# Kernel optimization log

Hardware: AMD Instinct MI355X
Metric: run time of the kernel (lower is better)

The kernel has to match this reference:

```python
import jax, jax.numpy as jnp
import numpy as np

# Instant-NGP multi-resolution hash grid constants (match init_kwargs)
L = 16            # num_levels
F = 2             # level_dim (features per level)
LOG2T = 19
T = 1 << LOG2T    # hashmap entries per level
BASE = 16.0       # base_resolution
SCALE = 1.3819061 # per_level_scale
HIDDEN = 64
N = 500_000
P1 = jnp.uint32(2654435761)  # NGP spatial hash primes (prime for dim0 is 1)
P2 = jnp.uint32(805459861)
# 8 corner offsets of the voxel, [8,3]
OFFS = jnp.array([[i, j, k] for i in (0, 1) for j in (0, 1) for k in (0, 1)], dtype=jnp.float32)


def hash_encode(x, table):
    # x: [N,3] in [0,1];  table: [L,T,F]
    res = jnp.floor(BASE * SCALE ** jnp.arange(L, dtype=jnp.float32))   # [L]
    pos = x[None] * (res[:, None, None] - 1.0)                          # [L,N,3]
    p0 = jnp.floor(pos)
    f = pos - p0                                                        # trilinear fracs [L,N,3]
    pi = p0.astype(jnp.uint32)                                          # [L,N,3]
    offs_u = OFFS.astype(jnp.uint32)                                    # [8,3]
    cx = pi[..., 0:1] + offs_u[None, None, :, 0]                        # [L,N,8]
    cy = pi[..., 1:2] + offs_u[None, None, :, 1]
    cz = pi[..., 2:3] + offs_u[None, None, :, 2]
    idx = (cx ^ (cy * P1) ^ (cz * P2)) & jnp.uint32(T - 1)              # [L,N,8] hashed table index
    feats = jax.vmap(lambda tab, i: tab[i])(table, idx)                 # per-level gather -> [L,N,8,F]
    # trilinear weights: prod over dims of (f if corner bit set else 1-f)
    w = jnp.prod(jnp.where(OFFS[None, None] > 0.5, f[:, :, None, :], 1.0 - f[:, :, None, :]), axis=-1)  # [L,N,8]
    out = jnp.einsum('lnc,lncf->lnf', w, feats)                         # [L,N,F]
    return out.transpose(1, 0, 2).reshape(x.shape[0], L * F)           # [N, L*F]


def setup_inputs() -> dict:
    key = jax.random.key(0)
    k = jax.random.split(key, 8)
    x = jax.random.uniform(k[0], (N, 3), dtype=jnp.float32)
    # NGP-style small uniform init for the hash tables
    table = jax.random.normal(k[1], (L, T, F), dtype=jnp.float32) * 1e-4
    feat_dim = L * F
    w1 = jax.random.normal(k[2], (feat_dim, HIDDEN), dtype=jnp.float32) / np.sqrt(feat_dim)
    b1 = jnp.zeros((HIDDEN,), jnp.float32)
    w2 = jax.random.normal(k[3], (HIDDEN, HIDDEN), dtype=jnp.float32) / np.sqrt(HIDDEN)
    b2 = jnp.zeros((HIDDEN,), jnp.float32)
    w3 = jax.random.normal(k[4], (HIDDEN, 3), dtype=jnp.float32) / np.sqrt(HIDDEN)
    b3 = jnp.zeros((3,), jnp.float32)
    return {"x": x, "table": table, "w1": w1, "b1": b1, "w2": w2, "b2": b2, "w3": w3, "b3": b3}


def reference(x, table, w1, b1, w2, b2, w3, b3):
    feat = hash_encode(x, table)                         # [N, 32]
    h = jax.nn.relu(feat @ w1 + b1)
    h = jax.nn.relu(h @ w2 + b2)
    rgb = jax.nn.sigmoid(h @ w3 + b3)                    # [N, 3]
    return rgb
```

## Files before the change

kernel.cpp:

```cpp
#include <hip/hip_runtime.h>
#include <hip/hip_fp16.h>
#include <math.h>


constexpr int      LVLS   = 16;
constexpr uint32_t TSIZE  = 1u << 19;
constexpr uint32_t TMASK  = TSIZE - 1u;
constexpr uint32_t PRIME1 = 2654435761u;
constexpr uint32_t PRIME2 = 805459861u;

struct ResArr { float v[LVLS]; };

typedef __attribute__((ext_vector_type(8))) short short8v;
typedef __attribute__((ext_vector_type(4))) float float4v;

__device__ inline ushort f2bf(float f) {
    uint u = __float_as_uint(f);
    u += 0x7fffu + ((u >> 16) & 1u);
    return (ushort)(u >> 16);
}

__device__ inline float2 h2f(uint u) {
    __half2 h = *reinterpret_cast<__half2*>(&u);
    return __half22float2(h);
}

__device__ inline uint pick4(const uint4& b, uint j) {
    const uint lo = (j & 1u) ? b.y : b.x;
    const uint hi = (j & 1u) ? b.w : b.z;
    return (j & 2u) ? hi : lo;
}

__global__ __launch_bounds__(256)
void ingp_conv(const float* __restrict__ table, uint* __restrict__ tab16,
               const float* __restrict__ x, float4* __restrict__ x4, int n)
{
    const int t = blockIdx.x * 256 + threadIdx.x;
    const int HALF = LVLS * (int)TSIZE / 2;
    if (t < HALF) {
        const float4 v = *reinterpret_cast<const float4*>(table + (size_t)t * 4u);
        __half2 ha = __floats2half2_rn(v.x, v.y);
        __half2 hb = __floats2half2_rn(v.z, v.w);
        uint2 o;
        o.x = *reinterpret_cast<uint*>(&ha);
        o.y = *reinterpret_cast<uint*>(&hb);
        *reinterpret_cast<uint2*>(tab16 + (size_t)t * 2u) = o;
    }
    if (t < n)
        x4[t] = make_float4(x[3 * t + 0], x[3 * t + 1], x[3 * t + 2], 0.f);
}

__global__ __launch_bounds__(256)
void ingp_prep(const float* __restrict__ w1, const float* __restrict__ w2,
               const float* __restrict__ w3,
               ushort* __restrict__ w1t, ushort* __restrict__ w2t,
               ushort* __restrict__ w3t)
{
    const int t = blockIdx.x * 256 + threadIdx.x;
    if (t < 2048) {
        const int nn = t >> 5, k = t & 31;
        w1t[t] = f2bf(w1[k * 64 + nn]);
    } else if (t < 2048 + 4096) {
        const int q = t - 2048;
        const int nn = q >> 6, k = q & 63;
        w2t[q] = f2bf(w2[k * 64 + nn]);
    } else if (t < 2048 + 4096 + 1024) {
        const int q = t - 6144;
        const int nn = q >> 6, k = q & 63;
        w3t[q] = (nn < 3) ? f2bf(w3[k * 3 + nn]) : (ushort)0;
    }
}

__global__ __launch_bounds__(256, 8)
void ingp_encode_f16(const float4* __restrict__ x4,
                     const uint* __restrict__ tab16,
                     uint* __restrict__ feat, int n, ResArr res)
{
    const int i = blockIdx.x * 256 + threadIdx.x;
    const int l = blockIdx.y;
    if (i >= n) return;

    const float4 xp = x4[i];
    const float rm1 = res.v[l];
    const float px = xp.x * rm1, py = xp.y * rm1, pz = xp.z * rm1;
    const float fpx = floorf(px), fpy = floorf(py), fpz = floorf(pz);
    const float fx = px - fpx, fy = py - fpy, fz = pz - fpz;
    const uint32_t ix = (uint32_t)fpx;
    const uint32_t iy = (uint32_t)fpy;
    const uint32_t iz = (uint32_t)fpz;
    const uint32_t hy0 = iy * PRIME1, hy1 = (iy + 1u) * PRIME1;
    const uint32_t hz0 = iz * PRIME2, hz1 = (iz + 1u) * PRIME2;
    const uint* tl = tab16 + (size_t)l * (size_t)TSIZE;

    uint32_t h0[4], h1[4];
    #pragma unroll
    for (int p = 0; p < 4; ++p) {
        const uint32_t bj = (p >> 1) & 1, bk = p & 1;
        const uint32_t hyz = (bj ? hy1 : hy0) ^ (bk ? hz1 : hz0);
        h0[p] = (ix ^ hyz) & TMASK;
        h1[p] = ((ix + 1u) ^ hyz) & TMASK;
    }

    uint e0[4], e1[4];
    if ((ix & 3u) != 3u) {
        #pragma unroll
        for (int p = 0; p < 4; ++p) {
            const uint32_t base = h0[p] & ~3u;
            const uint4 blk = *reinterpret_cast<const uint4*>(tl + base);
            e0[p] = pick4(blk, h0[p] & 3u);
            e1[p] = pick4(blk, h1[p] & 3u);
        }
    } else {
        #pragma unroll
        for (int p = 0; p < 4; ++p) {
            e0[p] = tl[h0[p]];
            e1[p] = tl[h1[p]];
        }
    }

    const float gx0 = 1.f - fx, gx1 = fx;
    float a0 = 0.f, a1 = 0.f;
    #pragma unroll
    for (int p = 0; p < 4; ++p) {
        const int bj = (p >> 1) & 1, bk = p & 1;
        const float wyz = (bj ? fy : 1.f - fy) * (bk ? fz : 1.f - fz);
        const float w0 = wyz * gx0, w1 = wyz * gx1;
        const float2 c0 = h2f(e0[p]);
        const float2 c1 = h2f(e1[p]);
        a0 = fmaf(w0, c0.x, a0);
        a1 = fmaf(w0, c0.y, a1);
        a0 = fmaf(w1, c1.x, a0);
        a1 = fmaf(w1, c1.y, a1);
    }
    feat[(size_t)l * n + i] = (uint)f2bf(a0) | ((uint)f2bf(a1) << 16);
}

__global__ __launch_bounds__(256, 8)
void ingp_encode(const float* __restrict__ x,
                 const float* __restrict__ table,
                 uint* __restrict__ feat, int n, ResArr res)
{
    const int i = blockIdx.x * 256 + threadIdx.x;
    const int l = blockIdx.y;
    if (i >= n) return;
    const float xx = x[3 * i + 0], xy = x[3 * i + 1], xz = x[3 * i + 2];
    const float rm1 = res.v[l];
    const float px = xx * rm1, py = xy * rm1, pz = xz * rm1;
    const float fpx = floorf(px), fpy = floorf(py), fpz = floorf(pz);
    const float fx = px - fpx, fy = py - fpy, fz = pz - fpz;
    const uint32_t ix = (uint32_t)fpx, iy = (uint32_t)fpy, iz = (uint32_t)fpz;
    const uint32_t hy0 = iy * PRIME1, hy1 = (iy + 1u) * PRIME1;
    const uint32_t hz0 = iz * PRIME2, hz1 = (iz + 1u) * PRIME2;
    const float* tl = table + (size_t)l * (size_t)TSIZE * 2u;

    uint32_t idx0[4], idx1[4];
    #pragma unroll
    for (int p = 0; p < 4; ++p) {
        const uint32_t bj = (p >> 1) & 1, bk = p & 1;
        const uint32_t hyz = (bj ? hy1 : hy0) ^ (bk ? hz1 : hz0);
        idx0[p] = (ix ^ hyz) & TMASK;
        idx1[p] = ((ix + 1u) ^ hyz) & TMASK;
    }
    float2 c0[4], c1[4];
    if ((ix & 1u) == 0u) {
        #pragma unroll
        for (int p = 0; p < 4; ++p) {
            const uint32_t base = idx0[p] & ~1u;
            const float4 q = *reinterpret_cast<const float4*>(tl + (size_t)base * 2u);
            if (idx0[p] & 1u) { c0[p] = make_float2(q.z, q.w); c1[p] = make_float2(q.x, q.y); }
            else              { c0[p] = make_float2(q.x, q.y); c1[p] = make_float2(q.z, q.w); }
        }
    } else {
        #pragma unroll
        for (int p = 0; p < 4; ++p) {
            c0[p] = *reinterpret_cast<const float2*>(tl + (size_t)idx0[p] * 2u);
            c1[p] = *reinterpret_cast<const float2*>(tl + (size_t)idx1[p] * 2u);
        }
    }
    const float gx0 = 1.f - fx, gx1 = fx;
    float a0 = 0.f, a1 = 0.f;
    #pragma unroll
    for (int p = 0; p < 4; ++p) {
        const int bj = (p >> 1) & 1, bk = p & 1;
        const float wyz = (bj ? fy : 1.f - fy) * (bk ? fz : 1.f - fz);
        const float w0 = wyz * gx0, w1 = wyz * gx1;
        a0 = fmaf(w0, c0[p].x, a0);
        a1 = fmaf(w0, c0[p].y, a1);
        a0 = fmaf(w1, c1[p].x, a0);
        a1 = fmaf(w1, c1[p].y, a1);
    }
    feat[(size_t)l * n + i] = (uint)f2bf(a0) | ((uint)f2bf(a1) << 16);
}

__global__ __launch_bounds__(256)
void ingp_mlp_mfma(const uint* __restrict__ feat,
                   const ushort* __restrict__ w1t,
                   const ushort* __restrict__ w2t,
                   const ushort* __restrict__ w3t,
                   const float* __restrict__ b1,
                   const float* __restrict__ b2,
                   const float* __restrict__ b3,
                   float* __restrict__ out, int n)
{
    __shared__ ushort s_h[4][64][72];
    const int tid = threadIdx.x;
    const int wv = tid >> 6;
    const int ln = tid & 63;
    const int lm = ln & 15;
    const int lk = ln >> 4;
    const int base = blockIdx.x * 256 + wv * 64;

    short8v a1[4];
    #pragma unroll
    for (int mt = 0; mt < 4; ++mt) {
        int pt = base + mt * 16 + lm;
        pt = pt < n ? pt : (n - 1);
        union { uint u[4]; short8v v; } c;
        #pragma unroll
        for (int j = 0; j < 4; ++j)
            c.u[j] = feat[(size_t)(lk * 4 + j) * (size_t)n + pt];
        a1[mt] = c.v;
    }

    float4v acc[4][4];
    #pragma unroll
    for (int nt = 0; nt < 4; ++nt) {
        const float bv = b1[nt * 16 + lm];
        #pragma unroll
        for (int mt = 0; mt < 4; ++mt)
            acc[mt][nt] = (float4v){bv, bv, bv, bv};
    }
    #pragma unroll
    for (int nt = 0; nt < 4; ++nt) {
        const short8v bfr = *(const short8v*)(w1t + (nt * 16 + lm) * 32 + lk * 8);
        #pragma unroll
        for (int mt = 0; mt < 4; ++mt)
            acc[mt][nt] = __builtin_amdgcn_mfma_f32_16x16x32_bf16(
                a1[mt], bfr, acc[mt][nt], 0, 0, 0);
    }
    #pragma unroll
    for (int mt = 0; mt < 4; ++mt)
        #pragma unroll
        for (int nt = 0; nt < 4; ++nt)
            #pragma unroll
            for (int r = 0; r < 4; ++r)
                s_h[wv][mt * 16 + lk * 4 + r][nt * 16 + lm] =
                    f2bf(fmaxf(acc[mt][nt][r], 0.f));
    __syncthreads();

    float4v acc2[4][4];
    #pragma unroll
    for (int nt = 0; nt < 4; ++nt) {
        const float bv = b2[nt * 16 + lm];
        #pragma unroll
        for (int mt = 0; mt < 4; ++mt)
            acc2[mt][nt] = (float4v){bv, bv, bv, bv};
    }
    #pragma unroll
    for (int ks = 0; ks < 2; ++ks) {
        short8v a2[4];
        #pragma unroll
        for (int mt = 0; mt < 4; ++mt)
            a2[mt] = *(const short8v*)&s_h[wv][mt * 16 + lm][ks * 32 + lk * 8];
        #pragma unroll
        for (int nt = 0; nt < 4; ++nt) {
            const short8v bfr =
                *(const short8v*)(w2t + (nt * 16 + lm) * 64 + ks * 32 + lk * 8);
            #pragma unroll
            for (int mt = 0; mt < 4; ++mt)
                acc2[mt][nt] = __builtin_amdgcn_mfma_f32_16x16x32_bf16(
                    a2[mt], bfr, acc2[mt][nt], 0, 0, 0);
        }
    }
    __syncthreads();
    #pragma unroll
    for (int mt = 0; mt < 4; ++mt)
        #pragma unroll
        for (int nt = 0; nt < 4; ++nt)
            #pragma unroll
            for (int r = 0; r < 4; ++r)
                s_h[wv][mt * 16 + lk * 4 + r][nt * 16 + lm] =
                    f2bf(fmaxf(acc2[mt][nt][r], 0.f));
    __syncthreads();

    float4v acc3[4];
    const float bv3 = (lm < 3) ? b3[lm] : 0.f;
    #pragma unroll
    for (int mt = 0; mt < 4; ++mt)
        acc3[mt] = (float4v){bv3, bv3, bv3, bv3};
    #pragma unroll
    for (int ks = 0; ks < 2; ++ks) {
        const short8v bfr = *(const short8v*)(w3t + lm * 64 + ks * 32 + lk * 8);
        #pragma unroll
        for (int mt = 0; mt < 4; ++mt) {
            const short8v a3 =
                *(const short8v*)&s_h[wv][mt * 16 + lm][ks * 32 + lk * 8];
            acc3[mt] = __builtin_amdgcn_mfma_f32_16x16x32_bf16(
                a3, bfr, acc3[mt], 0, 0, 0);
        }
    }
    if (lm < 3) {
        #pragma unroll
        for (int mt = 0; mt < 4; ++mt)
            #pragma unroll
            for (int r = 0; r < 4; ++r) {
                const int pt = base + mt * 16 + lk * 4 + r;
                if (pt < n)
                    out[pt * 3 + lm] = 1.f / (1.f + __expf(-acc3[mt][r]));
            }
    }
}

__global__ __launch_bounds__(256)
void ingp_mlp(const __half2* __restrict__ feat16,
              const float* __restrict__ w1, const float* __restrict__ b1,
              const float* __restrict__ w2, const float* __restrict__ b2,
              const float* __restrict__ w3, const float* __restrict__ b3,
              float* __restrict__ out, int n)
{
    __shared__ float s_w1[32 * 64];
    __shared__ float s_w2[64 * 64];
    __shared__ float s_w3[64 * 3];
    __shared__ float s_b1[64];
    __shared__ float s_b2[64];
    __shared__ float s_b3[3];
    for (int t = threadIdx.x; t < 32 * 64; t += 256) s_w1[t] = w1[t];
    for (int t = threadIdx.x; t < 64 * 64; t += 256) s_w2[t] = w2[t];
    for (int t = threadIdx.x; t < 64 * 3;  t += 256) s_w3[t] = w3[t];
    if (threadIdx.x < 64) { s_b1[threadIdx.x] = b1[threadIdx.x]; s_b2[threadIdx.x] = b2[threadIdx.x]; }
    if (threadIdx.x < 3) s_b3[threadIdx.x] = b3[threadIdx.x];
    __syncthreads();
    const int i = blockIdx.x * 256 + threadIdx.x;
    if (i >= n) return;
    float feat[32];
    #pragma unroll
    for (int l = 0; l < LVLS; ++l) {
        const float2 f = __half22float2(feat16[(size_t)l * n + i]);
        feat[2 * l + 0] = f.x;
        feat[2 * l + 1] = f.y;
    }
    float h1[64];
    #pragma unroll
    for (int j = 0; j < 64; ++j) h1[j] = s_b1[j];
    #pragma unroll
    for (int k = 0; k < 32; ++k) {
        const float fv = feat[k];
        #pragma unroll
        for (int j = 0; j < 64; ++j) h1[j] = fmaf(fv, s_w1[k * 64 + j], h1[j]);
    }
    #pragma unroll
    for (int j = 0; j < 64; ++j) h1[j] = fmaxf(h1[j], 0.f);
    float h2[64];
    #pragma unroll
    for (int j = 0; j < 64; ++j) h2[j] = s_b2[j];
    #pragma unroll
    for (int k = 0; k < 64; ++k) {
        const float hv = h1[k];
        #pragma unroll
        for (int j = 0; j < 64; ++j) h2[j] = fmaf(hv, s_w2[k * 64 + j], h2[j]);
    }
    #pragma unroll
    for (int j = 0; j < 64; ++j) h2[j] = fmaxf(h2[j], 0.f);
    float o0 = s_b3[0], o1 = s_b3[1], o2 = s_b3[2];
    #pragma unroll
    for (int j = 0; j < 64; ++j) {
        const float hv = h2[j];
        o0 = fmaf(hv, s_w3[j * 3 + 0], o0);
        o1 = fmaf(hv, s_w3[j * 3 + 1], o1);
        o2 = fmaf(hv, s_w3[j * 3 + 2], o2);
    }
    out[3 * i + 0] = 1.f / (1.f + __expf(-o0));
    out[3 * i + 1] = 1.f / (1.f + __expf(-o1));
    out[3 * i + 2] = 1.f / (1.f + __expf(-o2));
}

__global__ __launch_bounds__(256, 8)
void ingp_encode_h2(const float* __restrict__ x,
                    const float* __restrict__ table,
                    __half2* __restrict__ feat16, int n, ResArr res)
{
    const int i = blockIdx.x * 256 + threadIdx.x;
    const int l = blockIdx.y;
    if (i >= n) return;
    const float xx = x[3 * i + 0], xy = x[3 * i + 1], xz = x[3 * i + 2];
    const float rm1 = res.v[l];
    const float px = xx * rm1, py = xy * rm1, pz = xz * rm1;
    const float fpx = floorf(px), fpy = floorf(py), fpz = floorf(pz);
    const float fx = px - fpx, fy = py - fpy, fz = pz - fpz;
    const uint32_t ix = (uint32_t)fpx, iy = (uint32_t)fpy, iz = (uint32_t)fpz;
    const uint32_t hy0 = iy * PRIME1, hy1 = (iy + 1u) * PRIME1;
    const uint32_t hz0 = iz * PRIME2, hz1 = (iz + 1u) * PRIME2;
    const float* tl = table + (size_t)l * (size_t)TSIZE * 2u;
    float a0 = 0.f, a1 = 0.f;
    #pragma unroll
    for (int c = 0; c < 8; ++c) {
        const int bi = (c >> 2) & 1, bj = (c >> 1) & 1, bk = c & 1;
        const uint32_t h = ((ix + (uint32_t)bi) ^ (bj ? hy1 : hy0) ^ (bk ? hz1 : hz0)) & TMASK;
        const float2 tv = *reinterpret_cast<const float2*>(tl + (size_t)h * 2u);
        const float w = (bi ? fx : 1.f - fx) * (bj ? fy : 1.f - fy) * (bk ? fz : 1.f - fz);
        a0 = fmaf(w, tv.x, a0);
        a1 = fmaf(w, tv.y, a1);
    }
    feat16[(size_t)l * n + i] = __floats2half2_rn(a0, a1);
}

extern "C" void kernel_launch(void* const* d_in, const int* in_sizes, int n_in,
                              void* d_out, int out_size, void* d_ws, size_t ws_size,
                              hipStream_t stream)
{
    const float* x     = (const float*)d_in[0];
    const float* table = (const float*)d_in[1];
    const float* w1    = (const float*)d_in[2];
    const float* b1    = (const float*)d_in[3];
    const float* w2    = (const float*)d_in[4];
    const float* b2    = (const float*)d_in[5];
    const float* w3    = (const float*)d_in[6];
    const float* b3    = (const float*)d_in[7];
    float* out = (float*)d_out;

    const int n = in_sizes[0] / 3;

    ResArr res;
    const double S = (double)1.3819061f;
    double p = 1.0;
    for (int l = 0; l < LVLS; ++l) {
        res.v[l] = (float)floor(16.0 * p) - 1.0f;
        p *= S;
    }

    const int gb = (n + 255) / 256;
    const size_t feat_bytes = (size_t)LVLS * (size_t)n * 4u;
    const size_t tab16_bytes = (size_t)LVLS * (size_t)TSIZE * 4u;
    const size_t x4_bytes   = (size_t)n * 16u;

    const size_t off_tab16 = 16384;
    const size_t off_feat  = off_tab16 + tab16_bytes;
    const size_t off_x4    = off_feat + feat_bytes;
    const size_t need_full = off_x4 + x4_bytes;
    const size_t need_mid  = 16384 + feat_bytes;

    if (ws_size >= need_full) {
        ushort* w1t  = (ushort*)d_ws;
        ushort* w2t  = w1t + 2048;
        ushort* w3t  = w2t + 4096;
        uint*   tab16 = (uint*)((char*)d_ws + off_tab16);
        uint*   feat  = (uint*)((char*)d_ws + off_feat);
        float4* x4    = (float4*)((char*)d_ws + off_x4);

        const int conv_threads = LVLS * (int)TSIZE / 2;
        ingp_conv<<<(conv_threads + 255) / 256, 256, 0, stream>>>(
            table, tab16, x, x4, n);
        ingp_prep<<<28, 256, 0, stream>>>(w1, w2, w3, w1t, w2t, w3t);
        dim3 gridA(gb, LVLS);
        ingp_encode_f16<<<gridA, 256, 0, stream>>>(x4, tab16, feat, n, res);
        ingp_mlp_mfma<<<gb, 256, 0, stream>>>(feat, w1t, w2t, w3t,
                                              b1, b2, b3, out, n);
    } else if (ws_size >= need_mid) {
        ushort* w1t = (ushort*)d_ws;
        ushort* w2t = w1t + 2048;
        ushort* w3t = w2t + 4096;
        uint*   feat = (uint*)((char*)d_ws + 16384);
        ingp_prep<<<28, 256, 0, stream>>>(w1, w2, w3, w1t, w2t, w3t);
        dim3 gridA(gb, LVLS);
        ingp_encode<<<gridA, 256, 0, stream>>>(x, table, feat, n, res);
        ingp_mlp_mfma<<<gb, 256, 0, stream>>>(feat, w1t, w2t, w3t,
                                              b1, b2, b3, out, n);
    } else {
        dim3 gridA(gb, LVLS);
        ingp_encode_h2<<<gridA, 256, 0, stream>>>(x, table, (__half2*)d_ws, n, res);
        ingp_mlp<<<gb, 256, 0, stream>>>((const __half2*)d_ws,
                                         w1, b1, w2, b2, w3, b3, out, n);
    }
}
```

Baseline: 179.5 us.

## Spatially bin-sort input points before hash encoding to improve gather locality

Adds a counting sort of points into a 32^3 spatial grid (histogram, single-block scan, atomic scatter). The hash encoder then reads sorted points, and the MLP writes results back through a permutation. The aim is that neighbouring threads hit nearby table entries at coarse levels, which improves cache reuse for the random gathers. It also changes the gather so the aligned uint4 block load is always issued, with a scalar reload only for the wrap case. The cost is several extra launches, atomics, and scattered output writes.

```diff
diff --git a/kernel.cpp b/kernel.cpp
--- a/kernel.cpp
+++ b/kernel.cpp
@@ -8,6 +8,7 @@
 constexpr uint32_t TMASK  = TSIZE - 1u;
 constexpr uint32_t PRIME1 = 2654435761u;
 constexpr uint32_t PRIME2 = 805459861u;
+constexpr int      BINS   = 32768;
 
 struct ResArr { float v[LVLS]; };
 
@@ -29,6 +30,57 @@
     const uint lo = (j & 1u) ? b.y : b.x;
     const uint hi = (j & 1u) ? b.w : b.z;
     return (j & 2u) ? hi : lo;
+}
+
+__device__ inline uint skey(float X, float Y, float Z) {
+    uint kx = (uint)(X * 32.f); kx = kx > 31u ? 31u : kx;
+    uint ky = (uint)(Y * 32.f); ky = ky > 31u ? 31u : ky;
+    uint kz = (uint)(Z * 32.f); kz = kz > 31u ? 31u : kz;
+    return (kz << 10) | (ky << 5) | kx;
+}
+
+__global__ __launch_bounds__(256)
+void sort_hist(const float* __restrict__ x, uint* __restrict__ hist, int n)
+{
+    const int i = blockIdx.x * 256 + threadIdx.x;
+    if (i >= n) return;
+    atomicAdd(&hist[skey(x[3 * i], x[3 * i + 1], x[3 * i + 2])], 1u);
+}
+
+__global__ __launch_bounds__(256)
+void sort_scan(const uint* __restrict__ hist, uint* __restrict__ offs)
+{
+    __shared__ uint part[256];
+    const int t = threadIdx.x;
+    const int PER = BINS / 256;
+    uint s = 0;
+    for (int j = 0; j < PER; ++j) s += hist[t * PER + j];
+    part[t] = s;
+    __syncthreads();
+    for (int d = 1; d < 256; d <<= 1) {
+        uint v = (t >= d) ? part[t - d] : 0u;
+        __syncthreads();
+        part[t] += v;
+        __syncthreads();
+    }
+    uint base = (t == 0) ? 0u : part[t - 1];
+    for (int j = 0; j < PER; ++j) {
+        const uint h = hist[t * PER + j];
+        offs[t * PER + j] = base;
+        base += h;
+    }
+}
+
+__global__ __launch_bounds__(256)
+void sort_scatter(const float* __restrict__ x, uint* __restrict__ offs,
+                  float4* __restrict__ x4s, uint* __restrict__ perm, int n)
+{
+    const int i = blockIdx.x * 256 + threadIdx.x;
+    if (i >= n) return;
+    const float X = x[3 * i], Y = x[3 * i + 1], Z = x[3 * i + 2];
+    const uint pos = atomicAdd(&offs[skey(X, Y, Z)], 1u);
+    x4s[pos] = make_float4(X, Y, Z, 0.f);
+    perm[pos] = (uint)i;
 }
 
 __global__ __launch_bounds__(256)
@@ -101,21 +153,18 @@
         h1[p] = ((ix + 1u) ^ hyz) & TMASK;
     }
 
+    const bool fast = (ix & 3u) != 3u;
     uint e0[4], e1[4];
-    if ((ix & 3u) != 3u) {
-        #pragma unroll
-        for (int p = 0; p < 4; ++p) {
-            const uint32_t base = h0[p] & ~3u;
-            const uint4 blk = *reinterpret_cast<const uint4*>(tl + base);
-            e0[p] = pick4(blk, h0[p] & 3u);
-            e1[p] = pick4(blk, h1[p] & 3u);
-        }
-    } else {
-        #pragma unroll
-        for (int p = 0; p < 4; ++p) {
-            e0[p] = tl[h0[p]];
-            e1[p] = tl[h1[p]];
-        }
+    #pragma unroll
+    for (int p = 0; p < 4; ++p) {
+        const uint32_t base = h0[p] & ~3u;
+        const uint4 blk = *reinterpret_cast<const uint4*>(tl + base);
+        e0[p] = pick4(blk, h0[p] & 3u);
+        e1[p] = fast ? pick4(blk, h1[p] & 3u) : 0u;
+    }
+    if (!fast) {
+        #pragma unroll
+        for (int p = 0; p < 4; ++p) e1[p] = tl[h1[p]];
     }
 
     const float gx0 = 1.f - fx, gx1 = fx;
@@ -200,6 +249,7 @@
                    const float* __restrict__ b1,
                    const float* __restrict__ b2,
                    const float* __restrict__ b3,
+                   const uint* __restrict__ perm,
                    float* __restrict__ out, int n)
 {
     __shared__ ushort s_h[4][64][72];
@@ -305,8 +355,10 @@
             #pragma unroll
             for (int r = 0; r < 4; ++r) {
                 const int pt = base + mt * 16 + lk * 4 + r;
-                if (pt < n)
-                    out[pt * 3 + lm] = 1.f / (1.f + __expf(-acc3[mt][r]));
+                if (pt < n) {
+                    const uint o = perm ? perm[pt] : (uint)pt;
+                    out[o * 3u + lm] = 1.f / (1.f + __expf(-acc3[mt][r]));
+                }
             }
     }
 }
@@ -429,17 +481,47 @@
     }
 
     const int gb = (n + 255) / 256;
-    const size_t feat_bytes = (size_t)LVLS * (size_t)n * 4u;
+    const size_t feat_bytes  = (size_t)LVLS * (size_t)n * 4u;
     const size_t tab16_bytes = (size_t)LVLS * (size_t)TSIZE * 4u;
-    const size_t x4_bytes   = (size_t)n * 16u;
+    const size_t x4_bytes    = (size_t)n * 16u;
+    const size_t perm_bytes  = (size_t)n * 4u;
+    const size_t hist_bytes  = (size_t)BINS * 4u;
 
     const size_t off_tab16 = 16384;
     const size_t off_feat  = off_tab16 + tab16_bytes;
     const size_t off_x4    = off_feat + feat_bytes;
+    const size_t off_perm  = off_x4 + x4_bytes;
+    const size_t off_hist  = off_perm + perm_bytes;
+    const size_t off_offs  = off_hist + hist_bytes;
+    const size_t need_sort = off_offs + hist_bytes;
     const size_t need_full = off_x4 + x4_bytes;
     const size_t need_mid  = 16384 + feat_bytes;
 
-    if (ws_size >= need_full) {
+    if (ws_size >= need_sort) {
+        ushort* w1t  = (ushort*)d_ws;
+        ushort* w2t  = w1t + 2048;
+        ushort* w3t  = w2t + 4096;
+        uint*   tab16 = (uint*)((char*)d_ws + off_tab16);
+        uint*   feat  = (uint*)((char*)d_ws + off_feat);
+        float4* x4s   = (float4*)((char*)d_ws + off_x4);
+        uint*   perm  = (uint*)((char*)d_ws + off_perm);
+        uint*   hist  = (uint*)((char*)d_ws + off_hist);
+        uint*   offs  = (uint*)((char*)d_ws + off_offs);
+
+        hipMemsetAsync(hist, 0, hist_bytes, stream);
+        sort_hist<<<gb, 256, 0, stream>>>(x, hist, n);
+        sort_scan<<<1, 256, 0, stream>>>(hist, offs);
+        sort_scatter<<<gb, 256, 0, stream>>>(x, offs, x4s, perm, n);
+
+        const int conv_threads = LVLS * (int)TSIZE / 2;
+        ingp_conv<<<(conv_threads + 255) / 256, 256, 0, stream>>>(
+            table, tab16, x, (float4*)nullptr, 0);
+        ingp_prep<<<28, 256, 0, stream>>>(w1, w2, w3, w1t, w2t, w3t);
+        dim3 gridA(gb, LVLS);
+        ingp_encode_f16<<<gridA, 256, 0, stream>>>(x4s, tab16, feat, n, res);
+        ingp_mlp_mfma<<<gb, 256, 0, stream>>>(feat, w1t, w2t, w3t,
+                                              b1, b2, b3, perm, out, n);
+    } else if (ws_size >= need_full) {
         ushort* w1t  = (ushort*)d_ws;
         ushort* w2t  = w1t + 2048;
         ushort* w3t  = w2t + 4096;
@@ -454,7 +536,8 @@
         dim3 gridA(gb, LVLS);
         ingp_encode_f16<<<gridA, 256, 0, stream>>>(x4, tab16, feat, n, res);
         ingp_mlp_mfma<<<gb, 256, 0, stream>>>(feat, w1t, w2t, w3t,
-                                              b1, b2, b3, out, n);
+                                              b1, b2, b3, (const uint*)nullptr,
+                                              out, n);
     } else if (ws_size >= need_mid) {
         ushort* w1t = (ushort*)d_ws;
         ushort* w2t = w1t + 2048;
@@ -464,7 +547,8 @@
         dim3 gridA(gb, LVLS);
         ingp_encode<<<gridA, 256, 0, stream>>>(x, table, feat, n, res);
         ingp_mlp_mfma<<<gb, 256, 0, stream>>>(feat, w1t, w2t, w3t,
-                                              b1, b2, b3, out, n);
+                                              b1, b2, b3, (const uint*)nullptr,
+                                              out, n);
     } else {
         dim3 gridA(gb, LVLS);
         ingp_encode_h2<<<gridA, 256, 0, stream>>>(x, table, (__half2*)d_ws, n, res);
```

After: 238.6 us. +32.9%, slower.
